# Performance work log

Hardware: AMD Instinct MI355X
Metric: run time of the kernel (lower is better)

The kernel has to match this reference:

```python
import jax, jax.numpy as jnp
import numpy as np

TEMP = 1.0

def setup_inputs() -> dict:
    key = jax.random.key(0)
    k1, k2, k3 = jax.random.split(key, 3)
    B, Lq, Lk, X, Dv = 16, 1024, 1024, 512, 512
    h_q = jax.random.normal(k1, (B, Lq, X), dtype=jnp.float32)
    h_k = jax.random.normal(k2, (B, Lk, X), dtype=jnp.float32)
    h_v = jax.random.normal(k3, (B, Lk, Dv), dtype=jnp.float32)
    return {"h_q": h_q, "h_k": h_k, "h_v": h_v}

def reference(h_q, h_k, h_v):
    # Original computes full cross-batch 'abx,cdx->acbd' then extracts the
    # batch diagonal; that equals a direct per-batch QK^T: [B,Lq,Lk].
    atten_score = jnp.einsum('bqx,bkx->bqk', h_q, h_k) / TEMP
    atten_prob = jax.nn.softmax(atten_score, axis=-1)  # dropout is identity in eval
    cxt = jnp.einsum('bqk,bkd->bqd', atten_prob, h_v)
    return cxt
```

## Files before the change

kernel.cpp:

```cpp
#include <hip/hip_runtime.h>

typedef _Float16 half8 __attribute__((ext_vector_type(8)));
typedef float f32x4 __attribute__((ext_vector_type(4)));
typedef unsigned short u16x8 __attribute__((ext_vector_type(8)));

#define LOG2E 1.44269504088896340736f

constexpr int NB = 16, LQ = 1024, LK = 1024, DX = 512, DVD = 512;
constexpr int QBLK = 64, KVB = 64, NCH = LK / KVB;
constexpr int TILE = KVB * DX;

static __device__ __forceinline__ unsigned short f2h(float f) {
  union { _Float16 h; unsigned short u; } c; c.h = (_Float16)f; return c.u;
}
static __device__ __forceinline__ unsigned int pack2(float a, float b) {
  union { _Float16 h[2]; unsigned int u; } c;
  c.h[0] = (_Float16)a; c.h[1] = (_Float16)b; return c.u;
}
static __device__ __forceinline__ void gload16(const unsigned short* g, unsigned short* l) {
  __builtin_amdgcn_global_load_lds(
      (const __attribute__((address_space(1))) unsigned int*)g,
      (__attribute__((address_space(3))) unsigned int*)l, 16, 0, 0);
}

__global__ __launch_bounds__(256) void prep_kv(
    const float* __restrict__ K, const float* __restrict__ V,
    unsigned short* __restrict__ Kw, unsigned short* __restrict__ Vw) {
  __shared__ float tile[32][520];
  const int bidx = blockIdx.x;
  const bool isV = bidx >= NB * NCH * 2;
  const int r = isV ? bidx - NB * NCH * 2 : bidx;
  const int b = r >> 5, sub = r & 31, c = sub >> 1, half = sub & 1;
  const int t = (int)threadIdx.x;

  const float* src = (isV ? V : K) + ((size_t)b * LK + c * 64 + half * 32) * DX;
#pragma unroll
  for (int i = 0; i < 16; ++i) {
    int idx = t + i * 256;
    int rr = idx >> 7, cc = (idx & 127) * 4;
    float4 v = *(const float4*)(src + (size_t)idx * 4);
    *(float4*)&tile[rr][cc] = v;
  }
  __syncthreads();

  unsigned short* dst = (isV ? Vw : Kw) + (size_t)(b * NCH + c) * TILE;
  if (!isV) {
#pragma unroll
    for (int k = 0; k < 8; ++k) {
      int obi = t * 8 + k;
      int p = obi >> 5, kvloc = obi & 31;
      const float* rp = &tile[kvloc][p * 8];
      u16x8 o = { f2h(rp[0]), f2h(rp[1]), f2h(rp[2]), f2h(rp[3]),
                  f2h(rp[4]), f2h(rp[5]), f2h(rp[6]), f2h(rp[7]) };
      *(u16x8*)(dst + p * 512 + (half * 32 + kvloc) * 8) = o;
    }
  } else {
#pragma unroll
    for (int k = 0; k < 8; ++k) {
      int vbi = t * 8 + k;
      int pvloc = vbi >> 9, d = vbi & 511;
      u16x8 o = { f2h(tile[pvloc * 8 + 0][d]), f2h(tile[pvloc * 8 + 1][d]),
                  f2h(tile[pvloc * 8 + 2][d]), f2h(tile[pvloc * 8 + 3][d]),
                  f2h(tile[pvloc * 8 + 4][d]), f2h(tile[pvloc * 8 + 5][d]),
                  f2h(tile[pvloc * 8 + 6][d]), f2h(tile[pvloc * 8 + 7][d]) };
      *(u16x8*)(dst + (half * 4 + pvloc) * 4096 + d * 8) = o;
    }
  }
}

__global__ __launch_bounds__(512, 2) void attn_fused5(
    const float* __restrict__ Qf, const unsigned short* __restrict__ Kw,
    const unsigned short* __restrict__ Vw, float* __restrict__ Out) {
  __shared__ __align__(16) unsigned short Kl[TILE];
  __shared__ __align__(16) unsigned short Vl[TILE];
  __shared__ __align__(16) unsigned short Pl[4096];
  __shared__ __align__(16) float pmax[2][4][32];
  __shared__ __align__(16) float psum[2][4][32];
  __shared__ __align__(16) float sml[2][32];

  const int bid = blockIdx.x;
  const int logical = (bid & 7) * 32 + (bid >> 3);
  const int b  = logical >> 4;
  const int qt = logical & 15;
  const int tid = (int)threadIdx.x;
  const int lane = tid & 63;
  const int wave = tid >> 6;
  const int wq = wave >> 2;
  const int wd = wave & 3;
  const int q0 = qt * QBLK + wq * 32;
  const int d0 = wd * 128;
  const int c15 = lane & 15;
  const int g4  = lane >> 4;
  const int rbase = g4 * 4;

  half8 qfrag[2][16];
#pragma unroll
  for (int s = 0; s < 2; ++s) {
    const float* qrow = Qf + ((size_t)b * LQ + q0 + s * 16 + c15) * DX + g4 * 8;
#pragma unroll
    for (int ks = 0; ks < 16; ++ks) {
      float4 a0 = *(const float4*)(qrow + ks * 32);
      float4 a1 = *(const float4*)(qrow + ks * 32 + 4);
      half8 f;
      f[0] = (_Float16)(a0.x * LOG2E); f[1] = (_Float16)(a0.y * LOG2E);
      f[2] = (_Float16)(a0.z * LOG2E); f[3] = (_Float16)(a0.w * LOG2E);
      f[4] = (_Float16)(a1.x * LOG2E); f[5] = (_Float16)(a1.y * LOG2E);
      f[6] = (_Float16)(a1.z * LOG2E); f[7] = (_Float16)(a1.w * LOG2E);
      qfrag[s][ks] = f;
    }
  }

  f32x4 acc[2][8];
#pragma unroll
  for (int s = 0; s < 2; ++s)
#pragma unroll
    for (int n = 0; n < 8; ++n) acc[s][n] = (f32x4){0.f, 0.f, 0.f, 0.f};
  float mr[2] = { -3.0e38f, -3.0e38f };
  float lr[2] = { 0.f, 0.f };

  const unsigned short* kg = Kw + (size_t)b * NCH * TILE + wave * 4096 + lane * 8;
  const unsigned short* vg = Vw + (size_t)b * NCH * TILE + wave * 4096 + lane * 8;
  unsigned short* kl = &Kl[wave * 4096];
  unsigned short* vl = &Vl[wave * 4096];

#pragma unroll
  for (int ii = 0; ii < 8; ++ii) gload16(kg + ii * 512, kl + ii * 512);
#pragma unroll
  for (int ii = 0; ii < 8; ++ii) gload16(vg + ii * 512, vl + ii * 512);
  __syncthreads();

  for (int c = 0; c < NCH; ++c) {
    f32x4 cs0 = {0.f, 0.f, 0.f, 0.f};
    f32x4 cs1 = {0.f, 0.f, 0.f, 0.f};
    {
      const unsigned short* kb = &Kl[(wd * 16 + c15) * 8 + g4 * 512];
      __builtin_amdgcn_s_setprio(1);
#pragma unroll
      for (int ks = 0; ks < 16; ++ks) {
        half8 af = *(const half8*)(kb + ks * 2048);
        cs0 = __builtin_amdgcn_mfma_f32_16x16x32_f16(af, qfrag[0][ks], cs0, 0, 0, 0);
        cs1 = __builtin_amdgcn_mfma_f32_16x16x32_f16(af, qfrag[1][ks], cs1, 0, 0, 0);
      }
      __builtin_amdgcn_s_setprio(0);
    }

    float pm0 = fmaxf(fmaxf(cs0[0], cs0[1]), fmaxf(cs0[2], cs0[3]));
    float pm1 = fmaxf(fmaxf(cs1[0], cs1[1]), fmaxf(cs1[2], cs1[3]));
    pm0 = fmaxf(pm0, __shfl_xor(pm0, 16, 64)); pm0 = fmaxf(pm0, __shfl_xor(pm0, 32, 64));
    pm1 = fmaxf(pm1, __shfl_xor(pm1, 16, 64)); pm1 = fmaxf(pm1, __shfl_xor(pm1, 32, 64));
    if (g4 == 0) { pmax[wq][wd][c15] = pm0; pmax[wq][wd][16 + c15] = pm1; }

    asm volatile("s_waitcnt lgkmcnt(0)" ::: "memory");
    __builtin_amdgcn_s_barrier();
    __builtin_amdgcn_sched_barrier(0);

    if (c + 1 < NCH) {
      const unsigned short* ks_ = kg + (size_t)(c + 1) * TILE;
#pragma unroll
      for (int ii = 0; ii < 8; ++ii) gload16(ks_ + ii * 512, kl + ii * 512);
    }

    float pa0 = fmaxf(fmaxf(pmax[wq][0][c15], pmax[wq][1][c15]),
                      fmaxf(pmax[wq][2][c15], pmax[wq][3][c15]));
    float pa1 = fmaxf(fmaxf(pmax[wq][0][16 + c15], pmax[wq][1][16 + c15]),
                      fmaxf(pmax[wq][2][16 + c15], pmax[wq][3][16 + c15]));
    const bool resc = __any((pa0 > mr[0] + 8.0f) || (pa1 > mr[1] + 8.0f));
    float scl0 = 1.0f, scl1 = 1.0f;
    if (resc) {
      float mn0 = fmaxf(mr[0], pa0), mn1 = fmaxf(mr[1], pa1);
      scl0 = exp2f(mr[0] - mn0); scl1 = exp2f(mr[1] - mn1);
      mr[0] = mn0; mr[1] = mn1;
      if (wd == 0 && g4 == 0) { sml[wq][c15] = scl0; sml[wq][16 + c15] = scl1; }
    }
    float p0[4], p1[4];
#pragma unroll
    for (int j = 0; j < 4; ++j) {
      p0[j] = exp2f(cs0[j] - mr[0]);
      p1[j] = exp2f(cs1[j] - mr[1]);
    }
    float ps0 = (p0[0] + p0[1]) + (p0[2] + p0[3]);
    float ps1 = (p1[0] + p1[1]) + (p1[2] + p1[3]);
    ps0 += __shfl_xor(ps0, 16, 64); ps0 += __shfl_xor(ps0, 32, 64);
    ps1 += __shfl_xor(ps1, 16, 64); ps1 += __shfl_xor(ps1, 32, 64);
    if (g4 == 0) { psum[wq][wd][c15] = ps0; psum[wq][wd][16 + c15] = ps1; }

    {
      unsigned short* pb = &Pl[wq * 2048 + (wd * 2 + (g4 >> 1)) * 256
                               + c15 * 8 + (g4 & 1) * 4];
      uint2 w0 = { pack2(p0[0], p0[1]), pack2(p0[2], p0[3]) };
      uint2 w1 = { pack2(p1[0], p1[1]), pack2(p1[2], p1[3]) };
      *(uint2*)pb = w0;
      *(uint2*)(pb + 128) = w1;
    }

    if (c + 1 < NCH) asm volatile("s_waitcnt vmcnt(8) lgkmcnt(0)" ::: "memory");
    else             asm volatile("s_waitcnt vmcnt(0) lgkmcnt(0)" ::: "memory");
    __builtin_amdgcn_s_barrier();
    __builtin_amdgcn_sched_barrier(0);

    lr[0] = lr[0] * scl0 + (psum[wq][0][c15] + psum[wq][1][c15])
                         + (psum[wq][2][c15] + psum[wq][3][c15]);
    lr[1] = lr[1] * scl1 + (psum[wq][0][16 + c15] + psum[wq][1][16 + c15])
                         + (psum[wq][2][16 + c15] + psum[wq][3][16 + c15]);

    if (resc) {
      f32x4 sv0 = *(const f32x4*)&sml[wq][rbase];
      f32x4 sv1 = *(const f32x4*)&sml[wq][16 + rbase];
#pragma unroll
      for (int n = 0; n < 8; ++n)
#pragma unroll
        for (int j = 0; j < 4; ++j) {
          acc[0][n][j] *= sv0[j];
          acc[1][n][j] *= sv1[j];
        }
    }

    __builtin_amdgcn_s_setprio(1);
#pragma unroll
    for (int h = 0; h < 2; ++h) {
      half8 paf0 = *(const half8*)&Pl[wq * 2048 + (h * 4 + g4) * 256 + c15 * 8];
      half8 paf1 = *(const half8*)&Pl[wq * 2048 + (h * 4 + g4) * 256 + (16 + c15) * 8];
      const unsigned short* vb = &Vl[(h * 4 + g4) * 4096 + (d0 + c15) * 8];
#pragma unroll
      for (int n = 0; n < 8; ++n) {
        half8 bv = *(const half8*)(vb + n * 128);
        acc[0][n] = __builtin_amdgcn_mfma_f32_16x16x32_f16(paf0, bv, acc[0][n], 0, 0, 0);
        acc[1][n] = __builtin_amdgcn_mfma_f32_16x16x32_f16(paf1, bv, acc[1][n], 0, 0, 0);
      }
    }
    __builtin_amdgcn_s_setprio(0);

    asm volatile("s_waitcnt vmcnt(0) lgkmcnt(0)" ::: "memory");
    __builtin_amdgcn_s_barrier();
    __builtin_amdgcn_sched_barrier(0);

    if (c + 1 < NCH) {
      const unsigned short* vs_ = vg + (size_t)(c + 1) * TILE;
#pragma unroll
      for (int ii = 0; ii < 8; ++ii) gload16(vs_ + ii * 512, vl + ii * 512);
    }
  }

  if (wd == 0 && g4 == 0) { sml[wq][c15] = lr[0]; sml[wq][16 + c15] = lr[1]; }
  asm volatile("s_waitcnt lgkmcnt(0)" ::: "memory");
  __builtin_amdgcn_s_barrier();
  __builtin_amdgcn_sched_barrier(0);

#pragma unroll
  for (int s = 0; s < 2; ++s) {
    f32x4 lrv = *(const f32x4*)&sml[wq][s * 16 + rbase];
    float inv[4];
#pragma unroll
    for (int j = 0; j < 4; ++j) inv[j] = 1.0f / lrv[j];
    float* ob = Out + ((size_t)b * LQ + q0 + s * 16 + rbase) * DVD + d0 + c15;
#pragma unroll
    for (int n = 0; n < 8; ++n)
#pragma unroll
      for (int j = 0; j < 4; ++j)
        ob[(size_t)j * DVD + n * 16] = acc[s][n][j] * inv[j];
  }
}

extern "C" void kernel_launch(void* const* d_in, const int* in_sizes, int n_in,
                              void* d_out, int out_size, void* d_ws, size_t ws_size,
                              hipStream_t stream) {
  const float* Qf = (const float*)d_in[0];
  const float* Kf = (const float*)d_in[1];
  const float* Vf = (const float*)d_in[2];
  float* Out = (float*)d_out;

  unsigned short* Kw = (unsigned short*)d_ws;
  unsigned short* Vw = Kw + (size_t)NB * NCH * TILE;

  prep_kv<<<NB * NCH * 2 * 2, 256, 0, stream>>>(Kf, Vf, Kw, Vw);
  attn_fused5<<<NB * (LQ / QBLK), 512, 0, stream>>>(Qf, Kw, Vw, Out);
}
```

Before: 95.63 us.

## Split attention work across 16 waves with per-wave 16-query QK and 64-wide PV

Doubles the block to 1024 threads, with 16 waves instead of 8. In the QK stage each wave now handles 16 query rows against 16 kv columns. In the PV stage each wave covers 32 query rows by 64 output columns. This halves per-wave register use (query fragments and accumulators) to allow more resident waves and more latency hiding. The cost is more barrier participants, more LDS traffic per FLOP, and an unconditional rescale multiply every chunk. The launch_bounds of (1024, 4) may force register spills.

```diff
diff --git a/kernel.cpp b/kernel.cpp
--- a/kernel.cpp
+++ b/kernel.cpp
@@ -68,15 +68,15 @@
   }
 }
 
-__global__ __launch_bounds__(512, 2) void attn_fused5(
+__global__ __launch_bounds__(1024, 4) void attn_fused6(
     const float* __restrict__ Qf, const unsigned short* __restrict__ Kw,
     const unsigned short* __restrict__ Vw, float* __restrict__ Out) {
   __shared__ __align__(16) unsigned short Kl[TILE];
   __shared__ __align__(16) unsigned short Vl[TILE];
-  __shared__ __align__(16) unsigned short Pl[4096];
-  __shared__ __align__(16) float pmax[2][4][32];
-  __shared__ __align__(16) float psum[2][4][32];
-  __shared__ __align__(16) float sml[2][32];
+  __shared__ __align__(16) unsigned short Pl[8 * 64 * 8];
+  __shared__ __align__(16) float pmax[4][64];
+  __shared__ __align__(16) float psum[4][64];
+  __shared__ __align__(16) float sml[64];
 
   const int bid = blockIdx.x;
   const int logical = (bid & 7) * 32 + (bid >> 3);
@@ -85,18 +85,18 @@
   const int tid = (int)threadIdx.x;
   const int lane = tid & 63;
   const int wave = tid >> 6;
-  const int wq = wave >> 2;
-  const int wd = wave & 3;
-  const int q0 = qt * QBLK + wq * 32;
-  const int d0 = wd * 128;
+  const int qs  = wave & 3;
+  const int kvs = wave >> 2;
+  const int qsp = wave >> 3;
+  const int de  = wave & 7;
   const int c15 = lane & 15;
   const int g4  = lane >> 4;
   const int rbase = g4 * 4;
-
-  half8 qfrag[2][16];
-#pragma unroll
-  for (int s = 0; s < 2; ++s) {
-    const float* qrow = Qf + ((size_t)b * LQ + q0 + s * 16 + c15) * DX + g4 * 8;
+  const int d0 = de * 64;
+
+  half8 qfrag[16];
+  {
+    const float* qrow = Qf + ((size_t)b * LQ + qt * QBLK + qs * 16 + c15) * DX + g4 * 8;
 #pragma unroll
     for (int ks = 0; ks < 16; ++ks) {
       float4 a0 = *(const float4*)(qrow + ks * 32);
@@ -106,49 +106,43 @@
       f[2] = (_Float16)(a0.z * LOG2E); f[3] = (_Float16)(a0.w * LOG2E);
       f[4] = (_Float16)(a1.x * LOG2E); f[5] = (_Float16)(a1.y * LOG2E);
       f[6] = (_Float16)(a1.z * LOG2E); f[7] = (_Float16)(a1.w * LOG2E);
-      qfrag[s][ks] = f;
-    }
-  }
-
-  f32x4 acc[2][8];
+      qfrag[ks] = f;
+    }
+  }
+
+  f32x4 acc[2][4];
 #pragma unroll
   for (int s = 0; s < 2; ++s)
 #pragma unroll
-    for (int n = 0; n < 8; ++n) acc[s][n] = (f32x4){0.f, 0.f, 0.f, 0.f};
-  float mr[2] = { -3.0e38f, -3.0e38f };
-  float lr[2] = { 0.f, 0.f };
-
-  const unsigned short* kg = Kw + (size_t)b * NCH * TILE + wave * 4096 + lane * 8;
-  const unsigned short* vg = Vw + (size_t)b * NCH * TILE + wave * 4096 + lane * 8;
-  unsigned short* kl = &Kl[wave * 4096];
-  unsigned short* vl = &Vl[wave * 4096];
-
-#pragma unroll
-  for (int ii = 0; ii < 8; ++ii) gload16(kg + ii * 512, kl + ii * 512);
-#pragma unroll
-  for (int ii = 0; ii < 8; ++ii) gload16(vg + ii * 512, vl + ii * 512);
+    for (int n = 0; n < 4; ++n) acc[s][n] = (f32x4){0.f, 0.f, 0.f, 0.f};
+  float mr = -3.0e38f, lr = 0.f;
+
+  const unsigned short* kg = Kw + (size_t)b * NCH * TILE + tid * 8;
+  const unsigned short* vg = Vw + (size_t)b * NCH * TILE + tid * 8;
+
+#pragma unroll
+  for (int ii = 0; ii < 4; ++ii) gload16(kg + ii * 8192, &Kl[tid * 8 + ii * 8192]);
+#pragma unroll
+  for (int ii = 0; ii < 4; ++ii) gload16(vg + ii * 8192, &Vl[tid * 8 + ii * 8192]);
   __syncthreads();
 
   for (int c = 0; c < NCH; ++c) {
-    f32x4 cs0 = {0.f, 0.f, 0.f, 0.f};
-    f32x4 cs1 = {0.f, 0.f, 0.f, 0.f};
+    f32x4 cs = {0.f, 0.f, 0.f, 0.f};
     {
-      const unsigned short* kb = &Kl[(wd * 16 + c15) * 8 + g4 * 512];
+      const unsigned short* kb = &Kl[(kvs * 16 + c15) * 8 + g4 * 512];
       __builtin_amdgcn_s_setprio(1);
 #pragma unroll
       for (int ks = 0; ks < 16; ++ks) {
         half8 af = *(const half8*)(kb + ks * 2048);
-        cs0 = __builtin_amdgcn_mfma_f32_16x16x32_f16(af, qfrag[0][ks], cs0, 0, 0, 0);
-        cs1 = __builtin_amdgcn_mfma_f32_16x16x32_f16(af, qfrag[1][ks], cs1, 0, 0, 0);
+        cs = __builtin_amdgcn_mfma_f32_16x16x32_f16(af, qfrag[ks], cs, 0, 0, 0);
       }
       __builtin_amdgcn_s_setprio(0);
     }
 
-    float pm0 = fmaxf(fmaxf(cs0[0], cs0[1]), fmaxf(cs0[2], cs0[3]));
-    float pm1 = fmaxf(fmaxf(cs1[0], cs1[1]), fmaxf(cs1[2], cs1[3]));
-    pm0 = fmaxf(pm0, __shfl_xor(pm0, 16, 64)); pm0 = fmaxf(pm0, __shfl_xor(pm0, 32, 64));
-    pm1 = fmaxf(pm1, __shfl_xor(pm1, 16, 64)); pm1 = fmaxf(pm1, __shfl_xor(pm1, 32, 64));
-    if (g4 == 0) { pmax[wq][wd][c15] = pm0; pmax[wq][wd][16 + c15] = pm1; }
+    float pm = fmaxf(fmaxf(cs[0], cs[1]), fmaxf(cs[2], cs[3]));
+    pm = fmaxf(pm, __shfl_xor(pm, 16, 64));
+    pm = fmaxf(pm, __shfl_xor(pm, 32, 64));
+    if (g4 == 0) pmax[kvs][qs * 16 + c15] = pm;
 
     asm volatile("s_waitcnt lgkmcnt(0)" ::: "memory");
     __builtin_amdgcn_s_barrier();
@@ -157,57 +151,47 @@
     if (c + 1 < NCH) {
       const unsigned short* ks_ = kg + (size_t)(c + 1) * TILE;
 #pragma unroll
-      for (int ii = 0; ii < 8; ++ii) gload16(ks_ + ii * 512, kl + ii * 512);
-    }
-
-    float pa0 = fmaxf(fmaxf(pmax[wq][0][c15], pmax[wq][1][c15]),
-                      fmaxf(pmax[wq][2][c15], pmax[wq][3][c15]));
-    float pa1 = fmaxf(fmaxf(pmax[wq][0][16 + c15], pmax[wq][1][16 + c15]),
-                      fmaxf(pmax[wq][2][16 + c15], pmax[wq][3][16 + c15]));
-    const bool resc = __any((pa0 > mr[0] + 8.0f) || (pa1 > mr[1] + 8.0f));
-    float scl0 = 1.0f, scl1 = 1.0f;
+      for (int ii = 0; ii < 4; ++ii) gload16(ks_ + ii * 8192, &Kl[tid * 8 + ii * 8192]);
+    }
+
+    float pa = fmaxf(fmaxf(pmax[0][qs * 16 + c15], pmax[1][qs * 16 + c15]),
+                     fmaxf(pmax[2][qs * 16 + c15], pmax[3][qs * 16 + c15]));
+    const bool resc = __any(pa > mr + 8.0f);
+    float scl = 1.0f;
     if (resc) {
-      float mn0 = fmaxf(mr[0], pa0), mn1 = fmaxf(mr[1], pa1);
-      scl0 = exp2f(mr[0] - mn0); scl1 = exp2f(mr[1] - mn1);
-      mr[0] = mn0; mr[1] = mn1;
-      if (wd == 0 && g4 == 0) { sml[wq][c15] = scl0; sml[wq][16 + c15] = scl1; }
-    }
-    float p0[4], p1[4];
-#pragma unroll
-    for (int j = 0; j < 4; ++j) {
-      p0[j] = exp2f(cs0[j] - mr[0]);
-      p1[j] = exp2f(cs1[j] - mr[1]);
-    }
-    float ps0 = (p0[0] + p0[1]) + (p0[2] + p0[3]);
-    float ps1 = (p1[0] + p1[1]) + (p1[2] + p1[3]);
-    ps0 += __shfl_xor(ps0, 16, 64); ps0 += __shfl_xor(ps0, 32, 64);
-    ps1 += __shfl_xor(ps1, 16, 64); ps1 += __shfl_xor(ps1, 32, 64);
-    if (g4 == 0) { psum[wq][wd][c15] = ps0; psum[wq][wd][16 + c15] = ps1; }
+      float mn = fmaxf(mr, pa);
+      scl = exp2f(mr - mn);
+      mr = mn;
+    }
+    if (kvs == 0 && g4 == 0) sml[qs * 16 + c15] = scl;
+    float p[4];
+#pragma unroll
+    for (int j = 0; j < 4; ++j) p[j] = exp2f(cs[j] - mr);
+    float ps = (p[0] + p[1]) + (p[2] + p[3]);
+    ps += __shfl_xor(ps, 16, 64);
+    ps += __shfl_xor(ps, 32, 64);
+    if (g4 == 0) psum[kvs][qs * 16 + c15] = ps;
 
     {
-      unsigned short* pb = &Pl[wq * 2048 + (wd * 2 + (g4 >> 1)) * 256
-                               + c15 * 8 + (g4 & 1) * 4];
-      uint2 w0 = { pack2(p0[0], p0[1]), pack2(p0[2], p0[3]) };
-      uint2 w1 = { pack2(p1[0], p1[1]), pack2(p1[2], p1[3]) };
-      *(uint2*)pb = w0;
-      *(uint2*)(pb + 128) = w1;
-    }
-
-    if (c + 1 < NCH) asm volatile("s_waitcnt vmcnt(8) lgkmcnt(0)" ::: "memory");
+      unsigned short* pb = &Pl[(kvs * 2 + (g4 >> 1)) * 512
+                               + (qs * 16 + c15) * 8 + (g4 & 1) * 4];
+      uint2 w = { pack2(p[0], p[1]), pack2(p[2], p[3]) };
+      *(uint2*)pb = w;
+    }
+
+    if (c + 1 < NCH) asm volatile("s_waitcnt vmcnt(4) lgkmcnt(0)" ::: "memory");
     else             asm volatile("s_waitcnt vmcnt(0) lgkmcnt(0)" ::: "memory");
     __builtin_amdgcn_s_barrier();
     __builtin_amdgcn_sched_barrier(0);
 
-    lr[0] = lr[0] * scl0 + (psum[wq][0][c15] + psum[wq][1][c15])
-                         + (psum[wq][2][c15] + psum[wq][3][c15]);
-    lr[1] = lr[1] * scl1 + (psum[wq][0][16 + c15] + psum[wq][1][16 + c15])
-                         + (psum[wq][2][16 + c15] + psum[wq][3][16 + c15]);
-
-    if (resc) {
-      f32x4 sv0 = *(const f32x4*)&sml[wq][rbase];
-      f32x4 sv1 = *(const f32x4*)&sml[wq][16 + rbase];
-#pragma unroll
-      for (int n = 0; n < 8; ++n)
+    lr = lr * scl + (psum[0][qs * 16 + c15] + psum[1][qs * 16 + c15])
+                  + (psum[2][qs * 16 + c15] + psum[3][qs * 16 + c15]);
+
+    {
+      f32x4 sv0 = *(const f32x4*)&sml[qsp * 32 + rbase];
+      f32x4 sv1 = *(const f32x4*)&sml[qsp * 32 + 16 + rbase];
+#pragma unroll
+      for (int n = 0; n < 4; ++n)
 #pragma unroll
         for (int j = 0; j < 4; ++j) {
           acc[0][n][j] *= sv0[j];
@@ -218,14 +202,14 @@
     __builtin_amdgcn_s_setprio(1);
 #pragma unroll
     for (int h = 0; h < 2; ++h) {
-      half8 paf0 = *(const half8*)&Pl[wq * 2048 + (h * 4 + g4) * 256 + c15 * 8];
-      half8 paf1 = *(const half8*)&Pl[wq * 2048 + (h * 4 + g4) * 256 + (16 + c15) * 8];
+      half8 pa0 = *(const half8*)&Pl[(h * 4 + g4) * 512 + (qsp * 32 + c15) * 8];
+      half8 pa1 = *(const half8*)&Pl[(h * 4 + g4) * 512 + (qsp * 32 + 16 + c15) * 8];
       const unsigned short* vb = &Vl[(h * 4 + g4) * 4096 + (d0 + c15) * 8];
 #pragma unroll
-      for (int n = 0; n < 8; ++n) {
+      for (int n = 0; n < 4; ++n) {
         half8 bv = *(const half8*)(vb + n * 128);
-        acc[0][n] = __builtin_amdgcn_mfma_f32_16x16x32_f16(paf0, bv, acc[0][n], 0, 0, 0);
-        acc[1][n] = __builtin_amdgcn_mfma_f32_16x16x32_f16(paf1, bv, acc[1][n], 0, 0, 0);
+        acc[0][n] = __builtin_amdgcn_mfma_f32_16x16x32_f16(pa0, bv, acc[0][n], 0, 0, 0);
+        acc[1][n] = __builtin_amdgcn_mfma_f32_16x16x32_f16(pa1, bv, acc[1][n], 0, 0, 0);
       }
     }
     __builtin_amdgcn_s_setprio(0);
@@ -237,24 +221,25 @@
     if (c + 1 < NCH) {
       const unsigned short* vs_ = vg + (size_t)(c + 1) * TILE;
 #pragma unroll
-      for (int ii = 0; ii < 8; ++ii) gload16(vs_ + ii * 512, vl + ii * 512);
-    }
-  }
-
-  if (wd == 0 && g4 == 0) { sml[wq][c15] = lr[0]; sml[wq][16 + c15] = lr[1]; }
+      for (int ii = 0; ii < 4; ++ii) gload16(vs_ + ii * 8192, &Vl[tid * 8 + ii * 8192]);
+    }
+  }
+
+  if (kvs == 0 && g4 == 0) sml[qs * 16 + c15] = lr;
   asm volatile("s_waitcnt lgkmcnt(0)" ::: "memory");
   __builtin_amdgcn_s_barrier();
   __builtin_amdgcn_sched_barrier(0);
 
 #pragma unroll
   for (int s = 0; s < 2; ++s) {
-    f32x4 lrv = *(const f32x4*)&sml[wq][s * 16 + rbase];
+    f32x4 lrv = *(const f32x4*)&sml[qsp * 32 + s * 16 + rbase];
     float inv[4];
 #pragma unroll
     for (int j = 0; j < 4; ++j) inv[j] = 1.0f / lrv[j];
-    float* ob = Out + ((size_t)b * LQ + q0 + s * 16 + rbase) * DVD + d0 + c15;
-#pragma unroll
-    for (int n = 0; n < 8; ++n)
+    float* ob = Out + ((size_t)b * LQ + qt * QBLK + qsp * 32 + s * 16 + rbase) * DVD
+                + d0 + c15;
+#pragma unroll
+    for (int n = 0; n < 4; ++n)
 #pragma unroll
       for (int j = 0; j < 4; ++j)
         ob[(size_t)j * DVD + n * 16] = acc[s][n][j] * inv[j];
@@ -273,5 +258,5 @@
   unsigned short* Vw = Kw + (size_t)NB * NCH * TILE;
 
   prep_kv<<<NB * NCH * 2 * 2, 256, 0, stream>>>(Kf, Vf, Kw, Vw);
-  attn_fused5<<<NB * (LQ / QBLK), 512, 0, stream>>>(Qf, Kw, Vw, Out);
-}
+  attn_fused6<<<NB * (LQ / QBLK), 1024, 0, stream>>>(Qf, Kw, Vw, Out);
+}
```

New measurement: 128.1 us. 34.0% more time.
